# Kernel optimization log

Measured on AMD Instinct MI355X. Metric: run time of the kernel, lower is better.

The kernel has to match this reference:

```python
import jax, jax.numpy as jnp
import numpy as np

RADIUS = 8          # default radius in refine_mask_with_matting
EPS = 1e-05         # matting_eps
THRESH = 0.8        # threshold


def _box_filter(x, r):
    # F.avg_pool2d(kernel=2r+1, stride=1, padding=r) with count_include_pad=True:
    # zero-padded window sum divided by (2r+1)^2 everywhere (including borders).
    k = 2 * r + 1
    s = jax.lax.reduce_window(
        x, 0.0, jax.lax.add,
        window_dimensions=(1, 1, k, k),
        window_strides=(1, 1, 1, 1),
        padding=((0, 0), (0, 0), (r, r), (r, r)),
    )
    return s / (k * k)


def _guided_filter(guide, src, r, eps):
    # guide, src: [B,1,H,W]
    mean_I = _box_filter(guide, r)
    mean_p = _box_filter(src, r)
    mean_Ip = _box_filter(guide * src, r)
    cov_Ip = mean_Ip - mean_I * mean_p
    mean_II = _box_filter(guide * guide, r)
    var_I = mean_II - mean_I * mean_I
    a = cov_Ip / (var_I + eps)
    b = mean_p - a * mean_I
    mean_a = _box_filter(a, r)
    mean_b = _box_filter(b, r)
    return mean_a * guide + mean_b


def setup_inputs() -> dict:
    key = jax.random.key(0)
    k1, k2 = jax.random.split(key)
    B, C, H, W = 16, 3, 512, 512
    return {
        "output": jax.random.normal(k1, (B, C, H, W), dtype=jnp.float32),
        "input": jax.random.normal(k2, (B, C, H, W), dtype=jnp.float32),
    }


def reference(output, input):
    # --- Algorithm 1: light source map detection ---
    img = jnp.where(input.min() < 0, (input + 1.0) * 0.5, input)      # [B,3,H,W] in [0,1]
    max_intensity = jnp.max(img, axis=1, keepdims=True)                # [B,1,H,W]
    initial_mask = (max_intensity > THRESH).astype(img.dtype)          # [B,1,H,W]

    # matting refinement: guided filter with channel-mean guide (batched over B)
    guide = jnp.mean(img, axis=1, keepdims=True)                       # [B,1,H,W]
    refined = _guided_filter(guide, initial_mask, RADIUS, EPS)
    mask = jnp.clip(refined, 0.0, 1.0)                                 # [B,1,H,W]

    light_source = img * mask                                          # [B,3,H,W]

    # --- Eq. 2: L1 between masked output and light source ---
    output_01 = jnp.where(output.min() < 0, (output + 1.0) * 0.5, output)
    output_light_region = output_01 * mask
    loss = jnp.mean(jnp.abs(output_light_region - light_source))
    return loss
```

## Files before the change

### kernel.cpp

```cpp
#include <hip/hip_runtime.h>
#include <math.h>

#define BNUM 16
#define HNUM 512
#define WNUM 512
#define HW (HNUM*WNUM)
#define NPLANE (BNUM*HW)
#define RR 8
#define KWIN 17
#define EPSF 1e-5f
#define THRESHF 0.8f
#define STRIP 128
#define SEG_AB 32
#define SEG_ML 16
#define INV_KK (1.0f/289.0f)
#define INV_NUMEL (1.0f/12582912.0f)

__global__ __launch_bounds__(256) void prep_kernel(
        const float* __restrict__ outp, const float* __restrict__ inp,
        float* __restrict__ PI, float* __restrict__ PP, float* __restrict__ PS) {
    int pix = (blockIdx.x * 256 + threadIdx.x) * 4;
    if (pix >= NPLANE) return;
    int b = pix >> 18;
    int r = pix & (HW - 1);
    size_t base = (size_t)b * 3 * HW + r;

    float4 a0 = *(const float4*)(inp + base);
    float4 a1 = *(const float4*)(inp + base + HW);
    float4 a2 = *(const float4*)(inp + base + 2 * HW);
    float4 b0 = *(const float4*)(outp + base);
    float4 b1 = *(const float4*)(outp + base + HW);
    float4 b2 = *(const float4*)(outp + base + 2 * HW);

    float4 I4, P4, S4;
#define DOCOMP(M) { \
    float i0 = (a0.M + 1.f) * 0.5f; \
    float i1 = (a1.M + 1.f) * 0.5f; \
    float i2 = (a2.M + 1.f) * 0.5f; \
    I4.M = (i0 + i1 + i2) * (1.f/3.f); \
    float mx = fmaxf(i0, fmaxf(i1, i2)); \
    P4.M = (mx > THRESHF) ? 1.f : 0.f; \
    S4.M = 0.5f * (fabsf(b0.M - a0.M) + fabsf(b1.M - a1.M) + fabsf(b2.M - a2.M)); \
}
    DOCOMP(x) DOCOMP(y) DOCOMP(z) DOCOMP(w)
#undef DOCOMP

    size_t po = (size_t)b * HW + r;
    *(float4*)(PI + po) = I4;
    *(float4*)(PP + po) = P4;
    *(float4*)(PS + po) = S4;
}

__global__ __launch_bounds__(STRIP) void boxc_ab(
        const float* __restrict__ PI, const float* __restrict__ PP,
        float* __restrict__ PA, float* __restrict__ PB) {
    __shared__ float rowI[2][STRIP + 2 * RR];
    __shared__ float rowP[2][STRIP + 2 * RR];
    __shared__ float ring[4][KWIN][STRIP];

    int t  = threadIdx.x;
    int x0 = blockIdx.x * STRIP;
    int ys = blockIdx.y * SEG_AB;
    int b  = blockIdx.z;

    const float* Ib = PI + (size_t)b * HW;
    const float* Pb = PP + (size_t)b * HW;
    float* Ab = PA + (size_t)b * HW;
    float* Bb = PB + (size_t)b * HW;

    for (int i = t; i < 4 * KWIN * STRIP; i += STRIP) (&ring[0][0][0])[i] = 0.f;

    int xg  = x0 - RR + t;
    bool xok  = (xg >= 0) && (xg < WNUM);
    int xg2 = x0 - RR + STRIP + t;
    bool x2ok = (t < 2 * RR) && (xg2 < WNUM);

    float vI = 0.f, vP = 0.f, vIp = 0.f, vII = 0.f;
    int slot = 0;

    float ri0 = 0.f, rp0 = 0.f, ri1 = 0.f, rp1 = 0.f;
    {
        int y = ys - RR;
        if (y >= 0 && y < HNUM) {
            size_t ro = (size_t)y * WNUM;
            if (xok)  { ri0 = Ib[ro + xg];  rp0 = Pb[ro + xg]; }
            if (x2ok) { ri1 = Ib[ro + xg2]; rp1 = Pb[ro + xg2]; }
        }
    }

    int cur = 0;
    for (int k = 0; k < SEG_AB + 2 * RR; ++k) {
        int yin = ys - RR + k;
        rowI[cur][t] = ri0;
        rowP[cur][t] = rp0;
        if (t < 2 * RR) { rowI[cur][STRIP + t] = ri1; rowP[cur][STRIP + t] = rp1; }

        ri0 = 0.f; rp0 = 0.f; ri1 = 0.f; rp1 = 0.f;
        int yn = yin + 1;
        if (k + 1 < SEG_AB + 2 * RR && yn >= 0 && yn < HNUM) {
            size_t ro = (size_t)yn * WNUM;
            if (xok)  { ri0 = Ib[ro + xg];  rp0 = Pb[ro + xg]; }
            if (x2ok) { ri1 = Ib[ro + xg2]; rp1 = Pb[ro + xg2]; }
        }

        __syncthreads();

        float sI = 0.f, sP = 0.f, sIp = 0.f, sII = 0.f;
#pragma unroll
        for (int d = 0; d < KWIN; ++d) {
            float iv = rowI[cur][t + d];
            float pv = rowP[cur][t + d];
            sI  += iv;
            sP  += pv;
            sIp += iv * pv;
            sII += iv * iv;
        }

        vI  += sI  - ring[0][slot][t]; ring[0][slot][t] = sI;
        vP  += sP  - ring[1][slot][t]; ring[1][slot][t] = sP;
        vIp += sIp - ring[2][slot][t]; ring[2][slot][t] = sIp;
        vII += sII - ring[3][slot][t]; ring[3][slot][t] = sII;
        slot = (slot + 1 == KWIN) ? 0 : slot + 1;

        int yout = yin - RR;
        if (yout >= ys) {
            float mI  = vI  * INV_KK;
            float mP  = vP  * INV_KK;
            float mIp = vIp * INV_KK;
            float mII = vII * INV_KK;
            float cov = mIp - mI * mP;
            float var = mII - mI * mI;
            float a   = cov / (var + EPSF);
            float bb  = mP - a * mI;
            size_t off = (size_t)yout * WNUM + x0 + t;
            Ab[off] = a;
            Bb[off] = bb;
        }
        cur ^= 1;
    }
}

__global__ __launch_bounds__(STRIP) void boxc_mask_loss(
        const float* __restrict__ PA, const float* __restrict__ PB,
        const float* __restrict__ PI, const float* __restrict__ PS,
        float* __restrict__ loss_out) {
    __shared__ float rowA[2][STRIP + 2 * RR];
    __shared__ float rowB[2][STRIP + 2 * RR];
    __shared__ float ring[2][KWIN][STRIP];
    __shared__ float red[2];

    int t  = threadIdx.x;
    int x0 = blockIdx.x * STRIP;
    int ys = blockIdx.y * SEG_ML;
    int b  = blockIdx.z;

    const float* Ab = PA + (size_t)b * HW;
    const float* Bb = PB + (size_t)b * HW;
    const float* Ib = PI + (size_t)b * HW;
    const float* Sb = PS + (size_t)b * HW;

    for (int i = t; i < 2 * KWIN * STRIP; i += STRIP) (&ring[0][0][0])[i] = 0.f;

    int xg  = x0 - RR + t;
    bool xok  = (xg >= 0) && (xg < WNUM);
    int xg2 = x0 - RR + STRIP + t;
    bool x2ok = (t < 2 * RR) && (xg2 < WNUM);

    float vA = 0.f, vB = 0.f;
    int slot = 0;
    float partial = 0.f;

    float ra0 = 0.f, rb0 = 0.f, ra1 = 0.f, rb1 = 0.f;
    {
        int y = ys - RR;
        if (y >= 0 && y < HNUM) {
            size_t ro = (size_t)y * WNUM;
            if (xok)  { ra0 = Ab[ro + xg];  rb0 = Bb[ro + xg]; }
            if (x2ok) { ra1 = Ab[ro + xg2]; rb1 = Bb[ro + xg2]; }
        }
    }

    int cur = 0;
    for (int k = 0; k < SEG_ML + 2 * RR; ++k) {
        int yin = ys - RR + k;
        rowA[cur][t] = ra0;
        rowB[cur][t] = rb0;
        if (t < 2 * RR) { rowA[cur][STRIP + t] = ra1; rowB[cur][STRIP + t] = rb1; }

        ra0 = 0.f; rb0 = 0.f; ra1 = 0.f; rb1 = 0.f;
        int yn = yin + 1;
        if (k + 1 < SEG_ML + 2 * RR && yn >= 0 && yn < HNUM) {
            size_t ro = (size_t)yn * WNUM;
            if (xok)  { ra0 = Ab[ro + xg];  rb0 = Bb[ro + xg]; }
            if (x2ok) { ra1 = Ab[ro + xg2]; rb1 = Bb[ro + xg2]; }
        }

        __syncthreads();

        float sA = 0.f, sB = 0.f;
#pragma unroll
        for (int d = 0; d < KWIN; ++d) {
            sA += rowA[cur][t + d];
            sB += rowB[cur][t + d];
        }

        vA += sA - ring[0][slot][t]; ring[0][slot][t] = sA;
        vB += sB - ring[1][slot][t]; ring[1][slot][t] = sB;
        slot = (slot + 1 == KWIN) ? 0 : slot + 1;

        int yout = yin - RR;
        if (yout >= ys) {
            float mA = vA * INV_KK;
            float mB = vB * INV_KK;
            size_t off = (size_t)yout * WNUM + x0 + t;
            float refined = mA * Ib[off] + mB;
            float mask = fminf(fmaxf(refined, 0.f), 1.f);
            partial += mask * Sb[off];
        }
        cur ^= 1;
    }

#pragma unroll
    for (int off = 32; off > 0; off >>= 1)
        partial += __shfl_down(partial, off);
    if ((t & 63) == 0) red[t >> 6] = partial;
    __syncthreads();
    if (t == 0) atomicAdd(loss_out, (red[0] + red[1]) * INV_NUMEL);
}

extern "C" void kernel_launch(void* const* d_in, const int* in_sizes, int n_in,
                              void* d_out, int out_size, void* d_ws, size_t ws_size,
                              hipStream_t stream) {
    const float* outp = (const float*)d_in[0];
    const float* inp  = (const float*)d_in[1];

    float* ws = (float*)d_ws;
    float* PI = ws;
    float* PP = ws + (size_t)NPLANE;
    float* PS = ws + (size_t)2 * NPLANE;
    float* PA = ws + (size_t)3 * NPLANE;
    float* PB = ws + (size_t)4 * NPLANE;

    hipMemsetAsync(d_out, 0, sizeof(float), stream);

    prep_kernel<<<NPLANE / (256 * 4), 256, 0, stream>>>(outp, inp, PI, PP, PS);

    dim3 grid_ab(WNUM / STRIP, HNUM / SEG_AB, BNUM);
    boxc_ab<<<grid_ab, STRIP, 0, stream>>>(PI, PP, PA, PB);

    dim3 grid_ml(WNUM / STRIP, HNUM / SEG_ML, BNUM);
    boxc_mask_loss<<<grid_ml, STRIP, 0, stream>>>(PA, PB, PI, PS, (float*)d_out);
}
```

Measured before the change: 211.8 us.

## Batch rows per barrier and keep vertical ring buffers in registers

Both box-filter kernels now stage four rows per shared-memory step, so there are far fewer __syncthreads barriers, and the vertical running-sum ring buffers move from LDS into fully unrolled register arrays that shift each group. The AB kernel's vertical segment drops from 32 to 16 rows to match the mask kernel. That gives more blocks but raises halo recompute overhead from 1.5x to 2x of rows. Register pressure rises (4x17 ring floats plus prefetch arrays) in exchange for less LDS traffic and fewer barriers, and occupancy hints are added via launch_bounds.

```diff
diff --git a/kernel.cpp b/kernel.cpp
--- a/kernel.cpp
+++ b/kernel.cpp
@@ -11,8 +11,9 @@
 #define EPSF 1e-5f
 #define THRESHF 0.8f
 #define STRIP 128
-#define SEG_AB 32
-#define SEG_ML 16
+#define SEG 16
+#define RPG 4
+#define NGRP ((SEG + 2*RR) / RPG)
 #define INV_KK (1.0f/289.0f)
 #define INV_NUMEL (1.0f/12582912.0f)
 
@@ -51,16 +52,15 @@
     *(float4*)(PS + po) = S4;
 }
 
-__global__ __launch_bounds__(STRIP) void boxc_ab(
+__global__ __launch_bounds__(STRIP, 4) void boxc_ab(
         const float* __restrict__ PI, const float* __restrict__ PP,
         float* __restrict__ PA, float* __restrict__ PB) {
-    __shared__ float rowI[2][STRIP + 2 * RR];
-    __shared__ float rowP[2][STRIP + 2 * RR];
-    __shared__ float ring[4][KWIN][STRIP];
+    __shared__ float rowI[2][RPG][STRIP + 2 * RR];
+    __shared__ float rowP[2][RPG][STRIP + 2 * RR];
 
     int t  = threadIdx.x;
     int x0 = blockIdx.x * STRIP;
-    int ys = blockIdx.y * SEG_AB;
+    int ys = blockIdx.y * SEG;
     int b  = blockIdx.z;
 
     const float* Ib = PI + (size_t)b * HW;
@@ -68,90 +68,112 @@
     float* Ab = PA + (size_t)b * HW;
     float* Bb = PB + (size_t)b * HW;
 
-    for (int i = t; i < 4 * KWIN * STRIP; i += STRIP) (&ring[0][0][0])[i] = 0.f;
-
     int xg  = x0 - RR + t;
     bool xok  = (xg >= 0) && (xg < WNUM);
     int xg2 = x0 - RR + STRIP + t;
     bool x2ok = (t < 2 * RR) && (xg2 < WNUM);
 
+    float ringI[KWIN], ringP[KWIN], ringIp[KWIN], ringII[KWIN];
+#pragma unroll
+    for (int i = 0; i < KWIN; ++i) { ringI[i]=0.f; ringP[i]=0.f; ringIp[i]=0.f; ringII[i]=0.f; }
     float vI = 0.f, vP = 0.f, vIp = 0.f, vII = 0.f;
-    int slot = 0;
-
-    float ri0 = 0.f, rp0 = 0.f, ri1 = 0.f, rp1 = 0.f;
-    {
-        int y = ys - RR;
+
+    float pi0[RPG], pp0[RPG], pi1[RPG], pp1[RPG];
+#pragma unroll
+    for (int r = 0; r < RPG; ++r) {
+        pi0[r]=0.f; pp0[r]=0.f; pi1[r]=0.f; pp1[r]=0.f;
+        int y = ys - RR + r;
         if (y >= 0 && y < HNUM) {
             size_t ro = (size_t)y * WNUM;
-            if (xok)  { ri0 = Ib[ro + xg];  rp0 = Pb[ro + xg]; }
-            if (x2ok) { ri1 = Ib[ro + xg2]; rp1 = Pb[ro + xg2]; }
+            if (xok)  { pi0[r] = Ib[ro + xg];  pp0[r] = Pb[ro + xg]; }
+            if (x2ok) { pi1[r] = Ib[ro + xg2]; pp1[r] = Pb[ro + xg2]; }
         }
     }
 
     int cur = 0;
-    for (int k = 0; k < SEG_AB + 2 * RR; ++k) {
-        int yin = ys - RR + k;
-        rowI[cur][t] = ri0;
-        rowP[cur][t] = rp0;
-        if (t < 2 * RR) { rowI[cur][STRIP + t] = ri1; rowP[cur][STRIP + t] = rp1; }
-
-        ri0 = 0.f; rp0 = 0.f; ri1 = 0.f; rp1 = 0.f;
-        int yn = yin + 1;
-        if (k + 1 < SEG_AB + 2 * RR && yn >= 0 && yn < HNUM) {
-            size_t ro = (size_t)yn * WNUM;
-            if (xok)  { ri0 = Ib[ro + xg];  rp0 = Pb[ro + xg]; }
-            if (x2ok) { ri1 = Ib[ro + xg2]; rp1 = Pb[ro + xg2]; }
-        }
-
+    for (int g = 0; g < NGRP; ++g) {
+        int ybase = ys - RR + g * RPG;
+#pragma unroll
+        for (int r = 0; r < RPG; ++r) { rowI[cur][r][t] = pi0[r]; rowP[cur][r][t] = pp0[r]; }
+        if (t < 2 * RR) {
+#pragma unroll
+            for (int r = 0; r < RPG; ++r) { rowI[cur][r][STRIP+t] = pi1[r]; rowP[cur][r][STRIP+t] = pp1[r]; }
+        }
+#pragma unroll
+        for (int r = 0; r < RPG; ++r) { pi0[r]=0.f; pp0[r]=0.f; pi1[r]=0.f; pp1[r]=0.f; }
+        if (g + 1 < NGRP) {
+#pragma unroll
+            for (int r = 0; r < RPG; ++r) {
+                int y = ybase + RPG + r;
+                if (y >= 0 && y < HNUM) {
+                    size_t ro = (size_t)y * WNUM;
+                    if (xok)  { pi0[r] = Ib[ro + xg];  pp0[r] = Pb[ro + xg]; }
+                    if (x2ok) { pi1[r] = Ib[ro + xg2]; pp1[r] = Pb[ro + xg2]; }
+                }
+            }
+        }
         __syncthreads();
 
-        float sI = 0.f, sP = 0.f, sIp = 0.f, sII = 0.f;
-#pragma unroll
-        for (int d = 0; d < KWIN; ++d) {
-            float iv = rowI[cur][t + d];
-            float pv = rowP[cur][t + d];
-            sI  += iv;
-            sP  += pv;
-            sIp += iv * pv;
-            sII += iv * iv;
-        }
-
-        vI  += sI  - ring[0][slot][t]; ring[0][slot][t] = sI;
-        vP  += sP  - ring[1][slot][t]; ring[1][slot][t] = sP;
-        vIp += sIp - ring[2][slot][t]; ring[2][slot][t] = sIp;
-        vII += sII - ring[3][slot][t]; ring[3][slot][t] = sII;
-        slot = (slot + 1 == KWIN) ? 0 : slot + 1;
-
-        int yout = yin - RR;
-        if (yout >= ys) {
-            float mI  = vI  * INV_KK;
-            float mP  = vP  * INV_KK;
-            float mIp = vIp * INV_KK;
-            float mII = vII * INV_KK;
-            float cov = mIp - mI * mP;
-            float var = mII - mI * mI;
-            float a   = cov / (var + EPSF);
-            float bb  = mP - a * mI;
-            size_t off = (size_t)yout * WNUM + x0 + t;
-            Ab[off] = a;
-            Bb[off] = bb;
+        float sI[RPG], sP[RPG], sIp[RPG], sII[RPG];
+#pragma unroll
+        for (int r = 0; r < RPG; ++r) {
+            float aI=0.f, aP=0.f, aIp=0.f, aII=0.f;
+#pragma unroll
+            for (int d = 0; d < KWIN; ++d) {
+                float iv = rowI[cur][r][t + d];
+                float pv = rowP[cur][r][t + d];
+                aI += iv; aP += pv; aIp += iv * pv; aII += iv * iv;
+            }
+            sI[r]=aI; sP[r]=aP; sIp[r]=aIp; sII[r]=aII;
+        }
+
+        bool emit = (g >= (2 * RR) / RPG);
+#pragma unroll
+        for (int r = 0; r < RPG; ++r) {
+            vI  += sI[r]  - ringI[r];
+            vP  += sP[r]  - ringP[r];
+            vIp += sIp[r] - ringIp[r];
+            vII += sII[r] - ringII[r];
+            if (emit) {
+                int yout = ybase + r - RR;
+                float mI  = vI  * INV_KK;
+                float mP  = vP  * INV_KK;
+                float mIp = vIp * INV_KK;
+                float mII = vII * INV_KK;
+                float cov = mIp - mI * mP;
+                float var = mII - mI * mI;
+                float a   = cov / (var + EPSF);
+                float bb  = mP - a * mI;
+                size_t off = (size_t)yout * WNUM + x0 + t;
+                Ab[off] = a;
+                Bb[off] = bb;
+            }
+        }
+#pragma unroll
+        for (int i = 0; i < KWIN - RPG; ++i) {
+            ringI[i]=ringI[i+RPG]; ringP[i]=ringP[i+RPG];
+            ringIp[i]=ringIp[i+RPG]; ringII[i]=ringII[i+RPG];
+        }
+#pragma unroll
+        for (int r = 0; r < RPG; ++r) {
+            ringI[KWIN-RPG+r]=sI[r]; ringP[KWIN-RPG+r]=sP[r];
+            ringIp[KWIN-RPG+r]=sIp[r]; ringII[KWIN-RPG+r]=sII[r];
         }
         cur ^= 1;
     }
 }
 
-__global__ __launch_bounds__(STRIP) void boxc_mask_loss(
+__global__ __launch_bounds__(STRIP, 4) void boxc_mask_loss(
         const float* __restrict__ PA, const float* __restrict__ PB,
         const float* __restrict__ PI, const float* __restrict__ PS,
         float* __restrict__ loss_out) {
-    __shared__ float rowA[2][STRIP + 2 * RR];
-    __shared__ float rowB[2][STRIP + 2 * RR];
-    __shared__ float ring[2][KWIN][STRIP];
+    __shared__ float rowA[2][RPG][STRIP + 2 * RR];
+    __shared__ float rowB[2][RPG][STRIP + 2 * RR];
     __shared__ float red[2];
 
     int t  = threadIdx.x;
     int x0 = blockIdx.x * STRIP;
-    int ys = blockIdx.y * SEG_ML;
+    int ys = blockIdx.y * SEG;
     int b  = blockIdx.z;
 
     const float* Ab = PA + (size_t)b * HW;
@@ -159,64 +181,84 @@
     const float* Ib = PI + (size_t)b * HW;
     const float* Sb = PS + (size_t)b * HW;
 
-    for (int i = t; i < 2 * KWIN * STRIP; i += STRIP) (&ring[0][0][0])[i] = 0.f;
-
     int xg  = x0 - RR + t;
     bool xok  = (xg >= 0) && (xg < WNUM);
     int xg2 = x0 - RR + STRIP + t;
     bool x2ok = (t < 2 * RR) && (xg2 < WNUM);
 
+    float ringA[KWIN], ringB[KWIN];
+#pragma unroll
+    for (int i = 0; i < KWIN; ++i) { ringA[i]=0.f; ringB[i]=0.f; }
     float vA = 0.f, vB = 0.f;
-    int slot = 0;
     float partial = 0.f;
 
-    float ra0 = 0.f, rb0 = 0.f, ra1 = 0.f, rb1 = 0.f;
-    {
-        int y = ys - RR;
+    float pa0[RPG], pb0[RPG], pa1[RPG], pb1[RPG];
+#pragma unroll
+    for (int r = 0; r < RPG; ++r) {
+        pa0[r]=0.f; pb0[r]=0.f; pa1[r]=0.f; pb1[r]=0.f;
+        int y = ys - RR + r;
         if (y >= 0 && y < HNUM) {
             size_t ro = (size_t)y * WNUM;
-            if (xok)  { ra0 = Ab[ro + xg];  rb0 = Bb[ro + xg]; }
-            if (x2ok) { ra1 = Ab[ro + xg2]; rb1 = Bb[ro + xg2]; }
+            if (xok)  { pa0[r] = Ab[ro + xg];  pb0[r] = Bb[ro + xg]; }
+            if (x2ok) { pa1[r] = Ab[ro + xg2]; pb1[r] = Bb[ro + xg2]; }
         }
     }
 
     int cur = 0;
-    for (int k = 0; k < SEG_ML + 2 * RR; ++k) {
-        int yin = ys - RR + k;
-        rowA[cur][t] = ra0;
-        rowB[cur][t] = rb0;
-        if (t < 2 * RR) { rowA[cur][STRIP + t] = ra1; rowB[cur][STRIP + t] = rb1; }
-
-        ra0 = 0.f; rb0 = 0.f; ra1 = 0.f; rb1 = 0.f;
-        int yn = yin + 1;
-        if (k + 1 < SEG_ML + 2 * RR && yn >= 0 && yn < HNUM) {
-            size_t ro = (size_t)yn * WNUM;
-            if (xok)  { ra0 = Ab[ro + xg];  rb0 = Bb[ro + xg]; }
-            if (x2ok) { ra1 = Ab[ro + xg2]; rb1 = Bb[ro + xg2]; }
-        }
-
+    for (int g = 0; g < NGRP; ++g) {
+        int ybase = ys - RR + g * RPG;
+#pragma unroll
+        for (int r = 0; r < RPG; ++r) { rowA[cur][r][t] = pa0[r]; rowB[cur][r][t] = pb0[r]; }
+        if (t < 2 * RR) {
+#pragma unroll
+            for (int r = 0; r < RPG; ++r) { rowA[cur][r][STRIP+t] = pa1[r]; rowB[cur][r][STRIP+t] = pb1[r]; }
+        }
+#pragma unroll
+        for (int r = 0; r < RPG; ++r) { pa0[r]=0.f; pb0[r]=0.f; pa1[r]=0.f; pb1[r]=0.f; }
+        if (g + 1 < NGRP) {
+#pragma unroll
+            for (int r = 0; r < RPG; ++r) {
+                int y = ybase + RPG + r;
+                if (y >= 0 && y < HNUM) {
+                    size_t ro = (size_t)y * WNUM;
+                    if (xok)  { pa0[r] = Ab[ro + xg];  pb0[r] = Bb[ro + xg]; }
+                    if (x2ok) { pa1[r] = Ab[ro + xg2]; pb1[r] = Bb[ro + xg2]; }
+                }
+            }
+        }
         __syncthreads();
 
-        float sA = 0.f, sB = 0.f;
-#pragma unroll
-        for (int d = 0; d < KWIN; ++d) {
-            sA += rowA[cur][t + d];
-            sB += rowB[cur][t + d];
-        }
-
-        vA += sA - ring[0][slot][t]; ring[0][slot][t] = sA;
-        vB += sB - ring[1][slot][t]; ring[1][slot][t] = sB;
-        slot = (slot + 1 == KWIN) ? 0 : slot + 1;
-
-        int yout = yin - RR;
-        if (yout >= ys) {
-            float mA = vA * INV_KK;
-            float mB = vB * INV_KK;
-            size_t off = (size_t)yout * WNUM + x0 + t;
-            float refined = mA * Ib[off] + mB;
-            float mask = fminf(fmaxf(refined, 0.f), 1.f);
-            partial += mask * Sb[off];
-        }
+        float sA[RPG], sB[RPG];
+#pragma unroll
+        for (int r = 0; r < RPG; ++r) {
+            float aA=0.f, aB=0.f;
+#pragma unroll
+            for (int d = 0; d < KWIN; ++d) {
+                aA += rowA[cur][r][t + d];
+                aB += rowB[cur][r][t + d];
+            }
+            sA[r]=aA; sB[r]=aB;
+        }
+
+        bool emit = (g >= (2 * RR) / RPG);
+#pragma unroll
+        for (int r = 0; r < RPG; ++r) {
+            vA += sA[r] - ringA[r];
+            vB += sB[r] - ringB[r];
+            if (emit) {
+                int yout = ybase + r - RR;
+                float mA = vA * INV_KK;
+                float mB = vB * INV_KK;
+                size_t off = (size_t)yout * WNUM + x0 + t;
+                float refined = mA * Ib[off] + mB;
+                float mask = fminf(fmaxf(refined, 0.f), 1.f);
+                partial += mask * Sb[off];
+            }
+        }
+#pragma unroll
+        for (int i = 0; i < KWIN - RPG; ++i) { ringA[i]=ringA[i+RPG]; ringB[i]=ringB[i+RPG]; }
+#pragma unroll
+        for (int r = 0; r < RPG; ++r) { ringA[KWIN-RPG+r]=sA[r]; ringB[KWIN-RPG+r]=sB[r]; }
         cur ^= 1;
     }
 
@@ -245,9 +287,7 @@
 
     prep_kernel<<<NPLANE / (256 * 4), 256, 0, stream>>>(outp, inp, PI, PP, PS);
 
-    dim3 grid_ab(WNUM / STRIP, HNUM / SEG_AB, BNUM);
-    boxc_ab<<<grid_ab, STRIP, 0, stream>>>(PI, PP, PA, PB);
-
-    dim3 grid_ml(WNUM / STRIP, HNUM / SEG_ML, BNUM);
-    boxc_mask_loss<<<grid_ml, STRIP, 0, stream>>>(PA, PB, PI, PS, (float*)d_out);
-}
+    dim3 grid(WNUM / STRIP, HNUM / SEG, BNUM);
+    boxc_ab<<<grid, STRIP, 0, stream>>>(PI, PP, PA, PB);
+    boxc_mask_loss<<<grid, STRIP, 0, stream>>>(PA, PB, PI, PS, (float*)d_out);
+}
```

Result: slower. 501.2 us (+136.7%).
